# Optimization experiments

Hardware: AMD Instinct MI355X
Metric: run time of the kernel (lower is better)

Reference implementation:

```python
import jax, jax.numpy as jnp
import numpy as np

D_MODEL = 512
D_STATE = 16
D_CONV = 4
D_INNER = 2 * D_MODEL          # expand = 2 (mamba_ssm default)
DT_RANK = (D_MODEL + 15) // 16  # ceil(d_model/16) = 32
B, L = 2, 2048


def setup_inputs() -> dict:
    key = jax.random.key(0)
    ks = jax.random.split(key, 12)
    s = lambda k, shp, sc: jax.random.normal(k, shp, jnp.float32) * sc
    return {
        "x": s(ks[0], (B, L, D_MODEL), 1.0),
        "context": s(ks[1], (B, L, D_MODEL), 1.0),
        # Mamba params
        "in_proj_w": s(ks[2], (2 * D_INNER, D_MODEL), 0.02),
        "conv_w": s(ks[3], (D_INNER, D_CONV), 0.2),        # depthwise conv kernel
        "conv_b": jnp.zeros((D_INNER,), jnp.float32),
        "x_proj_w": s(ks[4], (DT_RANK + 2 * D_STATE, D_INNER), 0.02),
        "dt_proj_w": s(ks[5], (D_INNER, DT_RANK), 0.1),
        "dt_proj_b": s(ks[6], (D_INNER,), 0.1),
        "A_log": jnp.log(jnp.tile(jnp.arange(1, D_STATE + 1, dtype=jnp.float32), (D_INNER, 1))),
        "D": jnp.ones((D_INNER,), jnp.float32),
        "out_proj_w": s(ks[7], (D_MODEL, D_INNER), 0.02),
        # context gate params
        "gate_w": s(ks[8], (D_MODEL, 2 * D_MODEL), 0.02),
        "gate_b": jnp.zeros((D_MODEL,), jnp.float32),
    }


def _mamba(x, in_proj_w, conv_w, conv_b, x_proj_w, dt_proj_w, dt_proj_b, A_log, D, out_proj_w):
    Bsz, Ln, _ = x.shape
    # input projection -> [B, L, 2*E], split into ssm branch xi and gate z
    xz = jnp.einsum('bld,ed->ble', x, in_proj_w)
    xi, z = jnp.split(xz, 2, axis=-1)
    # causal depthwise conv1d (kernel D_CONV) + SiLU
    xp = jnp.pad(xi, ((0, 0), (D_CONV - 1, 0), (0, 0)))
    xc = sum(xp[:, k:k + Ln, :] * conv_w[:, k] for k in range(D_CONV)) + conv_b
    xc = jax.nn.silu(xc)
    # input-dependent dt, B, C
    dbc = jnp.einsum('ble,fe->blf', xc, x_proj_w)
    dt, Bm, Cm = jnp.split(dbc, [DT_RANK, DT_RANK + D_STATE], axis=-1)
    dt = jax.nn.softplus(jnp.einsum('blr,er->ble', dt, dt_proj_w) + dt_proj_b)  # [B,L,E]
    A = -jnp.exp(A_log)                                   # [E,S]
    dA = jnp.exp(dt[..., None] * A)                       # [B,L,E,S]
    dBx = dt[..., None] * Bm[:, :, None, :] * xc[..., None]  # [B,L,E,S]

    def step(h, ins):
        dA_t, dBx_t, C_t = ins
        h = dA_t * h + dBx_t                              # [B,E,S]
        y = jnp.einsum('bes,bs->be', h, C_t)
        return h, y

    h0 = jnp.zeros((Bsz, D_INNER, D_STATE), x.dtype)
    _, ys = jax.lax.scan(step, h0,
                         (dA.transpose(1, 0, 2, 3), dBx.transpose(1, 0, 2, 3), Cm.transpose(1, 0, 2)))
    y = ys.transpose(1, 0, 2) + xc * D                    # skip term D*x
    y = y * jax.nn.silu(z)                                # gated output
    return jnp.einsum('ble,de->bld', y, out_proj_w)


def reference(x, context, in_proj_w, conv_w, conv_b, x_proj_w, dt_proj_w, dt_proj_b,
              A_log, D, out_proj_w, gate_w, gate_b):
    m = _mamba(x, in_proj_w, conv_w, conv_b, x_proj_w, dt_proj_w, dt_proj_b, A_log, D, out_proj_w)
    g_in = jnp.concatenate([m, context], axis=-1)         # [B,L,2*d_model]
    gate = jax.nn.sigmoid(jnp.einsum('ble,de->bld', g_in, gate_w) + gate_b)
    return m * gate
```

## Files before the change

kernel.cpp:

```cpp
#include <hip/hip_runtime.h>
#include <cstdint>
#include <cstddef>

#define B_SZ   2
#define L_SZ   2048
#define BL     (B_SZ * L_SZ)
#define DMODEL 512
#define DINNER 1024
#define DSTATE 16
#define DTRANK 32
#define DTROWS 16
#define NCH    16
#define CHL    (L_SZ / NCH)

typedef unsigned short u16;
typedef __attribute__((ext_vector_type(8))) short          bf16x8;
typedef __attribute__((ext_vector_type(8))) unsigned short u16x8;
typedef __attribute__((ext_vector_type(4))) float          f32x4;

__device__ __forceinline__ void gload16(const void* g, void* l) {
    __builtin_amdgcn_global_load_lds(
        (const __attribute__((address_space(1))) unsigned int*)g,
        (__attribute__((address_space(3))) unsigned int*)l, 16, 0, 0);
}

__device__ __forceinline__ u16 bf16_rne(float x) {
    unsigned u = __float_as_uint(x);
    return (u16)((u + 0x7fffu + ((u >> 16) & 1u)) >> 16);
}

__global__ __launch_bounds__(256) void cvt_hl_k(
    const float* __restrict__ src, u16* __restrict__ hi, u16* __restrict__ lo,
    int shift, int dst_stride, int col_off)
{
    const long long base = ((long long)blockIdx.x * 256 + threadIdx.x) * 8;
    const long long row  = base >> shift;
    const int       col  = (int)(base & ((1 << shift) - 1));
    float4 f0 = *(const float4*)(src + base);
    float4 f1 = *(const float4*)(src + base + 4);
    float f[8] = {f0.x, f0.y, f0.z, f0.w, f1.x, f1.y, f1.z, f1.w};
    u16x8 h8, l8;
#pragma unroll
    for (int i = 0; i < 8; ++i) {
        u16 hb = bf16_rne(f[i]);
        float hf = __uint_as_float((unsigned)hb << 16);
        h8[i] = hb;
        l8[i] = bf16_rne(f[i] - hf);
    }
    const long long d = row * dst_stride + col_off + col;
    *(u16x8*)(hi + d) = h8;
    *(u16x8*)(lo + d) = l8;
}

template<int NF, int EPI>
__global__ __launch_bounds__(256) void gemm_bf16hl(
    const u16* __restrict__ Ah, const u16* __restrict__ Al,
    const u16* __restrict__ Wh, const u16* __restrict__ Wl,
    const float* __restrict__ bias, const float* __restrict__ Mul,
    float* __restrict__ C, float* __restrict__ C2, int M, int N, int K)
{
    constexpr int BN  = NF * 32;
    constexpr int NIB = BN / 16;
    constexpr int TOT = 16 + 2 * NIB;
    __shared__ u16 sAh[128][32], sAl[128][32];
    __shared__ u16 sBh[BN][32],  sBl[BN][32];

    const int tid  = threadIdx.x;
    const int w    = tid >> 6;
    const int lane = tid & 63;
    const int bm   = blockIdx.x * 128;
    const int bn   = blockIdx.y * BN;
    const int wm   = w >> 1;
    const int wn   = w & 1;
    const int lm   = lane & 15;
    const int lk8  = (lane >> 4) * 8;
    const int srow = lane >> 2;
    const int scol = (lane & 3) * 8;

    f32x4 acc[4][NF];
#pragma unroll
    for (int i = 0; i < 4; ++i)
#pragma unroll
        for (int j = 0; j < NF; ++j) acc[i][j] = (f32x4){0.f, 0.f, 0.f, 0.f};

    for (int k0 = 0; k0 < K; k0 += 32) {
        __syncthreads();
        for (int idx = w; idx < TOT; idx += 4) {
            const u16* gs; u16* ls;
            if (idx < 8)            { gs = Ah + (size_t)(bm + idx * 16 + srow) * K;              ls = &sAh[idx * 16][0]; }
            else if (idx < 16)      { gs = Al + (size_t)(bm + (idx - 8) * 16 + srow) * K;        ls = &sAl[(idx - 8) * 16][0]; }
            else if (idx < 16 + NIB){ gs = Wh + (size_t)(bn + (idx - 16) * 16 + srow) * K;       ls = &sBh[(idx - 16) * 16][0]; }
            else                    { gs = Wl + (size_t)(bn + (idx - 16 - NIB) * 16 + srow) * K; ls = &sBl[(idx - 16 - NIB) * 16][0]; }
            gload16(gs + k0 + scol, ls);
        }
        __syncthreads();

        bf16x8 a_h[4], a_l[4], b_h[NF], b_l[NF];
#pragma unroll
        for (int mi = 0; mi < 4; ++mi) {
            a_h[mi] = *(const bf16x8*)&sAh[wm * 64 + mi * 16 + lm][lk8];
            a_l[mi] = *(const bf16x8*)&sAl[wm * 64 + mi * 16 + lm][lk8];
        }
#pragma unroll
        for (int ni = 0; ni < NF; ++ni) {
            b_h[ni] = *(const bf16x8*)&sBh[wn * (NF * 16) + ni * 16 + lm][lk8];
            b_l[ni] = *(const bf16x8*)&sBl[wn * (NF * 16) + ni * 16 + lm][lk8];
        }
#pragma unroll
        for (int mi = 0; mi < 4; ++mi)
#pragma unroll
            for (int ni = 0; ni < NF; ++ni) {
                acc[mi][ni] = __builtin_amdgcn_mfma_f32_16x16x32_bf16(a_h[mi], b_h[ni], acc[mi][ni], 0, 0, 0);
                acc[mi][ni] = __builtin_amdgcn_mfma_f32_16x16x32_bf16(a_h[mi], b_l[ni], acc[mi][ni], 0, 0, 0);
                acc[mi][ni] = __builtin_amdgcn_mfma_f32_16x16x32_bf16(a_l[mi], b_h[ni], acc[mi][ni], 0, 0, 0);
            }
    }

    const int lr4 = (lane >> 4) * 4;
#pragma unroll
    for (int mi = 0; mi < 4; ++mi)
#pragma unroll
        for (int ni = 0; ni < NF; ++ni)
#pragma unroll
            for (int r = 0; r < 4; ++r) {
                const int row = bm + wm * 64 + mi * 16 + lr4 + r;
                const int col = bn + wn * (NF * 16) + ni * 16 + lm;
                if (EPI == 0) {
                    C[(size_t)row * N + col] = acc[mi][ni][r];
                } else if (EPI == 1) {
                    const size_t o = (size_t)row * N + col;
                    const float v = acc[mi][ni][r] + bias[col];
                    C[o] = Mul[o] / (1.f + expf(-v));
                } else {
                    if (col < DINNER) C [(size_t)row * DINNER + col]          = acc[mi][ni][r];
                    else              C2[(size_t)row * DINNER + col - DINNER] = acc[mi][ni][r];
                }
            }
}

__global__ __launch_bounds__(256) void gemm_xproj(
    const float* __restrict__ A, const float* __restrict__ W,
    float* __restrict__ C, int M, int N, int K)
{
    __shared__ float As[16][64];
    __shared__ float Ws[16][64];
    const int tid  = threadIdx.x;
    const int bm   = blockIdx.x * 64;
    const int tm   = (tid >> 4) * 4;
    const int tn   = (tid & 15) * 4;
    const int lrow = tid >> 2;
    const int lk   = (tid & 3) * 4;

    float acc[4][4];
#pragma unroll
    for (int i = 0; i < 4; ++i)
#pragma unroll
        for (int j = 0; j < 4; ++j) acc[i][j] = 0.f;

    for (int k0 = 0; k0 < K; k0 += 16) {
        const int kk = k0 + lk;
        float4 av = *(const float4*)(A + (size_t)(bm + lrow) * K + kk);
        float4 wv = *(const float4*)(W + (size_t)lrow * K + kk);
        __syncthreads();
        As[lk + 0][lrow] = av.x; As[lk + 1][lrow] = av.y;
        As[lk + 2][lrow] = av.z; As[lk + 3][lrow] = av.w;
        Ws[lk + 0][lrow] = wv.x; Ws[lk + 1][lrow] = wv.y;
        Ws[lk + 2][lrow] = wv.z; Ws[lk + 3][lrow] = wv.w;
        __syncthreads();
#pragma unroll
        for (int k = 0; k < 16; ++k) {
            float4 a4 = *(const float4*)&As[k][tm];
            float4 b4 = *(const float4*)&Ws[k][tn];
            float a[4] = {a4.x, a4.y, a4.z, a4.w};
            float b[4] = {b4.x, b4.y, b4.z, b4.w};
#pragma unroll
            for (int i = 0; i < 4; ++i)
#pragma unroll
                for (int j = 0; j < 4; ++j)
                    acc[i][j] = fmaf(a[i], b[j], acc[i][j]);
        }
    }
#pragma unroll
    for (int i = 0; i < 4; ++i)
        *(float4*)(C + (size_t)(bm + tm + i) * N + tn) =
            make_float4(acc[i][0], acc[i][1], acc[i][2], acc[i][3]);
}

__global__ __launch_bounds__(256) void conv_silu_k(
    const float* __restrict__ xi, const float* __restrict__ cw,
    const float* __restrict__ cb, float* __restrict__ xc)
{
    const int idx = blockIdx.x * 256 + threadIdx.x;
    const int e  = idx & (DINNER - 1);
    const int bl = idx >> 10;
    const int l  = bl & (L_SZ - 1);
    const float4 w = *(const float4*)(cw + e * 4);
    float acc = cb[e];
    acc = fmaf(xi[(size_t)bl * DINNER + e], w.w, acc);
    if (l >= 1) acc = fmaf(xi[(size_t)(bl - 1) * DINNER + e], w.z, acc);
    if (l >= 2) acc = fmaf(xi[(size_t)(bl - 2) * DINNER + e], w.y, acc);
    if (l >= 3) acc = fmaf(xi[(size_t)(bl - 3) * DINNER + e], w.x, acc);
    xc[idx] = acc / (1.f + expf(-acc));
}

__global__ __launch_bounds__(256) void dt_softplus_k(
    const float* __restrict__ dbc, const float* __restrict__ Wdt,
    const float* __restrict__ bdt, float* __restrict__ dt)
{
    __shared__ float r[DTROWS][DTRANK];
    const int rb  = blockIdx.x * DTROWS;
    const int tid = threadIdx.x;
    for (int i = tid; i < DTROWS * DTRANK; i += 256)
        r[i >> 5][i & 31] = dbc[(size_t)(rb + (i >> 5)) * 64 + (i & 31)];
    __syncthreads();
    for (int n = tid; n < DINNER; n += 256) {
        float4 wv[8];
        const float* w = Wdt + (size_t)n * DTRANK;
#pragma unroll
        for (int q = 0; q < 8; ++q) wv[q] = *(const float4*)(w + q * 4);
        const float bn_ = bdt[n];
#pragma unroll
        for (int row = 0; row < DTROWS; ++row) {
            float acc = bn_;
#pragma unroll
            for (int q = 0; q < 8; ++q) {
                acc = fmaf(wv[q].x, r[row][q * 4 + 0], acc);
                acc = fmaf(wv[q].y, r[row][q * 4 + 1], acc);
                acc = fmaf(wv[q].z, r[row][q * 4 + 2], acc);
                acc = fmaf(wv[q].w, r[row][q * 4 + 3], acc);
            }
            dt[(size_t)(rb + row) * DINNER + n] = (acc > 20.f) ? acc : log1pf(expf(acc));
        }
    }
}


__global__ __launch_bounds__(128) void scan_p1(
    const float* __restrict__ dtb, const float* __restrict__ xc,
    const float* __restrict__ dbc, const float* __restrict__ A_log,
    float* __restrict__ Pst, float* __restrict__ Hst)
{
    const int bid = blockIdx.x;
    const int c  = bid & (NCH - 1);
    const int eg = (bid >> 4) & 127;
    const int b  = bid >> 11;
    const int tid = threadIdx.x;
    const int el = tid >> 4, s = tid & 15;
    const int e  = eg * 8 + el;

    const float Av = -expf(A_log[e * DSTATE + s]);
    const size_t base = (size_t)b * L_SZ + c * CHL;
    float h = 0.f, P = 1.f;

    float dtv = dtb[base * DINNER + e];
    float xcv = xc [base * DINNER + e];
    float Bv  = dbc[base * 64 + DTRANK + s];
    for (int l = 0; l < CHL; ++l) {
        float dt_n = 0.f, xc_n = 0.f, B_n = 0.f;
        if (l + 1 < CHL) {
            const size_t r = base + l + 1;
            dt_n = dtb[r * DINNER + e];
            xc_n = xc [r * DINNER + e];
            B_n  = dbc[r * 64 + DTRANK + s];
        }
        const float dA = expf(dtv * Av);
        h = fmaf(dA, h, dtv * Bv * xcv);
        P *= dA;
        dtv = dt_n; xcv = xc_n; Bv = B_n;
    }
    const size_t off = (((size_t)c * B_SZ + b) * DINNER + e) * DSTATE + s;
    Pst[off] = P;
    Hst[off] = h;
}

__global__ __launch_bounds__(256) void scan_comb(
    const float* __restrict__ Pst, float* __restrict__ Hst)
{
    const int idx = blockIdx.x * 256 + threadIdx.x;
    float h = 0.f;
    for (int c = 0; c < NCH; ++c) {
        const size_t off = (size_t)c * (B_SZ * DINNER * DSTATE) + idx;
        const float P = Pst[off];
        const float H = Hst[off];
        Hst[off] = h;
        h = fmaf(P, h, H);
    }
}

__global__ __launch_bounds__(128) void scan_p2(
    const float* __restrict__ dtb, const float* __restrict__ xc,
    const float* __restrict__ z, const float* __restrict__ dbc,
    const float* __restrict__ A_log, const float* __restrict__ Dp,
    const float* __restrict__ H0,
    u16* __restrict__ y_hi, u16* __restrict__ y_lo)
{
    const int bid = blockIdx.x;
    const int c  = bid & (NCH - 1);
    const int eg = (bid >> 4) & 127;
    const int b  = bid >> 11;
    const int tid = threadIdx.x;
    const int el = tid >> 4, s = tid & 15;
    const int e  = eg * 8 + el;

    const float Av = -expf(A_log[e * DSTATE + s]);
    const float Dv = Dp[e];
    const size_t base = (size_t)b * L_SZ + c * CHL;
    float h = H0[(((size_t)c * B_SZ + b) * DINNER + e) * DSTATE + s];

    float dtv = dtb[base * DINNER + e];
    float xcv = xc [base * DINNER + e];
    float Bv  = dbc[base * 64 + DTRANK + s];
    float Cv  = dbc[base * 64 + DTRANK + DSTATE + s];
    float zv  = z  [base * DINNER + e];
    for (int l = 0; l < CHL; ++l) {
        float dt_n = 0.f, xc_n = 0.f, B_n = 0.f, C_n = 0.f, z_n = 0.f;
        if (l + 1 < CHL) {
            const size_t r = base + l + 1;
            dt_n = dtb[r * DINNER + e];
            xc_n = xc [r * DINNER + e];
            B_n  = dbc[r * 64 + DTRANK + s];
            C_n  = dbc[r * 64 + DTRANK + DSTATE + s];
            z_n  = z  [r * DINNER + e];
        }
        h = fmaf(expf(dtv * Av), h, dtv * Bv * xcv);
        float yp = h * Cv;
        yp += __shfl_xor(yp, 1, 16);
        yp += __shfl_xor(yp, 2, 16);
        yp += __shfl_xor(yp, 4, 16);
        yp += __shfl_xor(yp, 8, 16);
        if (s == 0) {
            const float sg = zv / (1.f + expf(-zv));
            const float yv = fmaf(xcv, Dv, yp) * sg;
            const u16 hb = bf16_rne(yv);
            const float hf = __uint_as_float((unsigned)hb << 16);
            const size_t o = (base + l) * DINNER + e;
            y_hi[o] = hb;
            y_lo[o] = bf16_rne(yv - hf);
        }
        dtv = dt_n; xcv = xc_n; Bv = B_n; Cv = C_n; zv = z_n;
    }
}

extern "C" void kernel_launch(void* const* d_in, const int* in_sizes, int n_in,
                              void* d_out, int out_size, void* d_ws, size_t ws_size,
                              hipStream_t stream)
{
    const float* x         = (const float*)d_in[0];
    const float* context   = (const float*)d_in[1];
    const float* in_proj_w = (const float*)d_in[2];
    const float* conv_w    = (const float*)d_in[3];
    const float* conv_b    = (const float*)d_in[4];
    const float* x_proj_w  = (const float*)d_in[5];
    const float* dt_proj_w = (const float*)d_in[6];
    const float* dt_proj_b = (const float*)d_in[7];
    const float* A_log     = (const float*)d_in[8];
    const float* Dvec      = (const float*)d_in[9];
    const float* out_proj_w= (const float*)d_in[10];
    const float* gate_w    = (const float*)d_in[11];
    const float* gate_b    = (const float*)d_in[12];
    float* out = (float*)d_out;

    char* wsb = (char*)d_ws;
    float* xi   = (float*)(wsb + (size_t)( 0u << 20));
    float* z    = (float*)(wsb + (size_t)(16u << 20));
    float* xc   = (float*)(wsb + (size_t)(32u << 20));
    float* dbc  = (float*)(wsb + (size_t)(48u << 20));
    float* dt   = (float*)(wsb + (size_t)(49u << 20));
    float* m    = (float*)(wsb + (size_t)(65u << 20));
    u16* x_hi   = (u16*)(wsb + (size_t)(65u << 20));
    u16* x_lo   = (u16*)(wsb + (size_t)(69u << 20));
    u16* Wi_hi  = (u16*)(wsb + (size_t)(73u << 20));
    u16* Wi_lo  = (u16*)(wsb + (size_t)(75u << 20));
    float* Pst  = (float*)(wsb + (size_t)(73u << 20));
    float* Hst  = (float*)(wsb + (size_t)(75u << 20));
    u16* Wo_hi  = (u16*)(wsb + (size_t)(77u << 20));
    u16* Wo_lo  = (u16*)(wsb + (size_t)(78u << 20));
    u16* Wg_hi  = (u16*)(wsb + (size_t)(79u << 20));
    u16* Wg_lo  = (u16*)(wsb + (size_t)(80u << 20));
    u16* y_hi   = (u16*)(wsb + (size_t)( 0u << 20));
    u16* y_lo   = (u16*)(wsb + (size_t)( 8u << 20));
    u16* A7_hi  = (u16*)(wsb + (size_t)(16u << 20));
    u16* A7_lo  = (u16*)(wsb + (size_t)(24u << 20));

    cvt_hl_k<<<1024, 256, 0, stream>>>(x,          x_hi,  x_lo,   9,  512, 0);
    cvt_hl_k<<< 512, 256, 0, stream>>>(in_proj_w,  Wi_hi, Wi_lo,  9,  512, 0);
    cvt_hl_k<<< 256, 256, 0, stream>>>(out_proj_w, Wo_hi, Wo_lo, 10, 1024, 0);
    cvt_hl_k<<< 256, 256, 0, stream>>>(gate_w,     Wg_hi, Wg_lo, 10, 1024, 0);
    gemm_bf16hl<4, 2><<<dim3(BL / 128, 2048 / 128), 256, 0, stream>>>(
        x_hi, x_lo, Wi_hi, Wi_lo, nullptr, nullptr, xi, z, BL, 2048, DMODEL);
    conv_silu_k<<<(BL * DINNER) / 256, 256, 0, stream>>>(xi, conv_w, conv_b, xc);
    gemm_xproj<<<dim3(BL / 64, 1), 256, 0, stream>>>(xc, x_proj_w, dbc, BL, 64, DINNER);
    dt_softplus_k<<<BL / DTROWS, 256, 0, stream>>>(dbc, dt_proj_w, dt_proj_b, dt);
    scan_p1<<<B_SZ * 128 * NCH, 128, 0, stream>>>(dt, xc, dbc, A_log, Pst, Hst);
    scan_comb<<<(B_SZ * DINNER * DSTATE) / 256, 256, 0, stream>>>(Pst, Hst);
    scan_p2<<<B_SZ * 128 * NCH, 128, 0, stream>>>(dt, xc, z, dbc, A_log, Dvec, Hst,
                                                  y_hi, y_lo);
    gemm_bf16hl<2, 0><<<dim3(BL / 128, DMODEL / 64), 256, 0, stream>>>(
        y_hi, y_lo, Wo_hi, Wo_lo, nullptr, nullptr, m, nullptr, BL, DMODEL, DINNER);
    cvt_hl_k<<<1024, 256, 0, stream>>>(m,       A7_hi, A7_lo, 9, 1024, 0);
    cvt_hl_k<<<1024, 256, 0, stream>>>(context, A7_hi, A7_lo, 9, 1024, DMODEL);
    gemm_bf16hl<2, 1><<<dim3(BL / 128, DMODEL / 64), 256, 0, stream>>>(
        A7_hi, A7_lo, Wg_hi, Wg_lo, gate_b, m, out, nullptr, BL, DMODEL, 2 * DMODEL);
}
```

Before: 484.6 us.

## Restructure chunked scan: 8 states per thread, more chunks, closed-form chunk decay

Rewrites both scan passes so each thread owns 8 state entries of one channel instead of one, with 128 channels per block. Loads of B and C become float4 vectors and the y reduction needs only one shuffle. The chunk count is doubled to keep the grid filled. Pass 1 computes the chunk decay product as exp2 of A times the summed dt rather than a running product, and exp is replaced by exp2 with a pre-scaled A. This cuts redundant per-lane loads of dt, xc and z and the shuffle work, at the cost of more registers per thread and twice the data for the combine step.

```diff
diff --git a/kernel.cpp b/kernel.cpp
--- a/kernel.cpp
+++ b/kernel.cpp
@@ -10,7 +10,7 @@
 #define DSTATE 16
 #define DTRANK 32
 #define DTROWS 16
-#define NCH    16
+#define NCH    32
 #define CHL    (L_SZ / NCH)
 
 typedef unsigned short u16;
@@ -235,42 +235,61 @@
 }
 
 
-__global__ __launch_bounds__(128) void scan_p1(
+__global__ __launch_bounds__(256) void scan_p1(
     const float* __restrict__ dtb, const float* __restrict__ xc,
     const float* __restrict__ dbc, const float* __restrict__ A_log,
     float* __restrict__ Pst, float* __restrict__ Hst)
 {
     const int bid = blockIdx.x;
-    const int c  = bid & (NCH - 1);
-    const int eg = (bid >> 4) & 127;
-    const int b  = bid >> 11;
+    const int c   = bid & (NCH - 1);
+    const int eg  = (bid >> 5) & 7;
+    const int b   = bid >> 8;
     const int tid = threadIdx.x;
-    const int el = tid >> 4, s = tid & 15;
-    const int e  = eg * 8 + el;
-
-    const float Av = -expf(A_log[e * DSTATE + s]);
-    const size_t base = (size_t)b * L_SZ + c * CHL;
-    float h = 0.f, P = 1.f;
-
-    float dtv = dtb[base * DINNER + e];
-    float xcv = xc [base * DINNER + e];
-    float Bv  = dbc[base * 64 + DTRANK + s];
+    const int e    = eg * 128 + (tid >> 1);
+    const int s0   = (tid & 1) * 8;
+
+    float A2[8];
+    {
+        float4 a0 = *(const float4*)(A_log + e * DSTATE + s0);
+        float4 a1 = *(const float4*)(A_log + e * DSTATE + s0 + 4);
+        const float c2 = 1.44269504088896f;
+        A2[0] = -expf(a0.x) * c2; A2[1] = -expf(a0.y) * c2;
+        A2[2] = -expf(a0.z) * c2; A2[3] = -expf(a0.w) * c2;
+        A2[4] = -expf(a1.x) * c2; A2[5] = -expf(a1.y) * c2;
+        A2[6] = -expf(a1.z) * c2; A2[7] = -expf(a1.w) * c2;
+    }
+    float h[8] = {0.f, 0.f, 0.f, 0.f, 0.f, 0.f, 0.f, 0.f};
+    float dtsum = 0.f;
+    const size_t base = (size_t)b * L_SZ + (size_t)c * CHL;
+    const float* dtp = dtb + base * DINNER + e;
+    const float* xcp = xc  + base * DINNER + e;
+    const float* dbp = dbc + base * 64 + DTRANK + s0;
+    float dtv = *dtp, xcv = *xcp;
+
     for (int l = 0; l < CHL; ++l) {
-        float dt_n = 0.f, xc_n = 0.f, B_n = 0.f;
-        if (l + 1 < CHL) {
-            const size_t r = base + l + 1;
-            dt_n = dtb[r * DINNER + e];
-            xc_n = xc [r * DINNER + e];
-            B_n  = dbc[r * 64 + DTRANK + s];
-        }
-        const float dA = expf(dtv * Av);
-        h = fmaf(dA, h, dtv * Bv * xcv);
-        P *= dA;
-        dtv = dt_n; xcv = xc_n; Bv = B_n;
-    }
-    const size_t off = (((size_t)c * B_SZ + b) * DINNER + e) * DSTATE + s;
-    Pst[off] = P;
-    Hst[off] = h;
+        float4 B0 = *(const float4*)(dbp);
+        float4 B1 = *(const float4*)(dbp + 4);
+        const size_t adv = (l + 1 < CHL) ? DINNER : 0;
+        float dt_n = dtp[adv];
+        float xc_n = xcp[adv];
+        dtsum += dtv;
+        const float u = dtv * xcv;
+        const float Bs[8] = {B0.x, B0.y, B0.z, B0.w, B1.x, B1.y, B1.z, B1.w};
+#pragma unroll
+        for (int j = 0; j < 8; ++j) {
+            const float dA = exp2f(dtv * A2[j]);
+            h[j] = fmaf(dA, h[j], Bs[j] * u);
+        }
+        dtv = dt_n; xcv = xc_n;
+        dtp += DINNER; xcp += DINNER; dbp += 64;
+    }
+    const size_t off = (((size_t)c * B_SZ + b) * DINNER + e) * DSTATE + s0;
+    *(float4*)(Pst + off)     = make_float4(exp2f(A2[0] * dtsum), exp2f(A2[1] * dtsum),
+                                            exp2f(A2[2] * dtsum), exp2f(A2[3] * dtsum));
+    *(float4*)(Pst + off + 4) = make_float4(exp2f(A2[4] * dtsum), exp2f(A2[5] * dtsum),
+                                            exp2f(A2[6] * dtsum), exp2f(A2[7] * dtsum));
+    *(float4*)(Hst + off)     = make_float4(h[0], h[1], h[2], h[3]);
+    *(float4*)(Hst + off + 4) = make_float4(h[4], h[5], h[6], h[7]);
 }
 
 __global__ __launch_bounds__(256) void scan_comb(
@@ -287,7 +306,7 @@
     }
 }
 
-__global__ __launch_bounds__(128) void scan_p2(
+__global__ __launch_bounds__(256) void scan_p2(
     const float* __restrict__ dtb, const float* __restrict__ xc,
     const float* __restrict__ z, const float* __restrict__ dbc,
     const float* __restrict__ A_log, const float* __restrict__ Dp,
@@ -295,49 +314,68 @@
     u16* __restrict__ y_hi, u16* __restrict__ y_lo)
 {
     const int bid = blockIdx.x;
-    const int c  = bid & (NCH - 1);
-    const int eg = (bid >> 4) & 127;
-    const int b  = bid >> 11;
+    const int c   = bid & (NCH - 1);
+    const int eg  = (bid >> 5) & 7;
+    const int b   = bid >> 8;
     const int tid = threadIdx.x;
-    const int el = tid >> 4, s = tid & 15;
-    const int e  = eg * 8 + el;
-
-    const float Av = -expf(A_log[e * DSTATE + s]);
+    const int e    = eg * 128 + (tid >> 1);
+    const int half = tid & 1;
+    const int s0   = half * 8;
+
+    float A2[8];
+    {
+        float4 a0 = *(const float4*)(A_log + e * DSTATE + s0);
+        float4 a1 = *(const float4*)(A_log + e * DSTATE + s0 + 4);
+        const float c2 = 1.44269504088896f;
+        A2[0] = -expf(a0.x) * c2; A2[1] = -expf(a0.y) * c2;
+        A2[2] = -expf(a0.z) * c2; A2[3] = -expf(a0.w) * c2;
+        A2[4] = -expf(a1.x) * c2; A2[5] = -expf(a1.y) * c2;
+        A2[6] = -expf(a1.z) * c2; A2[7] = -expf(a1.w) * c2;
+    }
     const float Dv = Dp[e];
-    const size_t base = (size_t)b * L_SZ + c * CHL;
-    float h = H0[(((size_t)c * B_SZ + b) * DINNER + e) * DSTATE + s];
-
-    float dtv = dtb[base * DINNER + e];
-    float xcv = xc [base * DINNER + e];
-    float Bv  = dbc[base * 64 + DTRANK + s];
-    float Cv  = dbc[base * 64 + DTRANK + DSTATE + s];
-    float zv  = z  [base * DINNER + e];
+    const size_t base = (size_t)b * L_SZ + (size_t)c * CHL;
+    const size_t hoff = (((size_t)c * B_SZ + b) * DINNER + e) * DSTATE + s0;
+    float h[8];
+    {
+        float4 h0 = *(const float4*)(H0 + hoff);
+        float4 h1 = *(const float4*)(H0 + hoff + 4);
+        h[0] = h0.x; h[1] = h0.y; h[2] = h0.z; h[3] = h0.w;
+        h[4] = h1.x; h[5] = h1.y; h[6] = h1.z; h[7] = h1.w;
+    }
+    const float* dtp = dtb + base * DINNER + e;
+    const float* xcp = xc  + base * DINNER + e;
+    const float* zp  = z   + base * DINNER + e;
+    const float* dbp = dbc + base * 64 + DTRANK + s0;
+    float dtv = *dtp, xcv = *xcp, zv = *zp;
+
     for (int l = 0; l < CHL; ++l) {
-        float dt_n = 0.f, xc_n = 0.f, B_n = 0.f, C_n = 0.f, z_n = 0.f;
-        if (l + 1 < CHL) {
-            const size_t r = base + l + 1;
-            dt_n = dtb[r * DINNER + e];
-            xc_n = xc [r * DINNER + e];
-            B_n  = dbc[r * 64 + DTRANK + s];
-            C_n  = dbc[r * 64 + DTRANK + DSTATE + s];
-            z_n  = z  [r * DINNER + e];
-        }
-        h = fmaf(expf(dtv * Av), h, dtv * Bv * xcv);
-        float yp = h * Cv;
-        yp += __shfl_xor(yp, 1, 16);
-        yp += __shfl_xor(yp, 2, 16);
-        yp += __shfl_xor(yp, 4, 16);
-        yp += __shfl_xor(yp, 8, 16);
-        if (s == 0) {
-            const float sg = zv / (1.f + expf(-zv));
-            const float yv = fmaf(xcv, Dv, yp) * sg;
-            const u16 hb = bf16_rne(yv);
-            const float hf = __uint_as_float((unsigned)hb << 16);
-            const size_t o = (base + l) * DINNER + e;
-            y_hi[o] = hb;
-            y_lo[o] = bf16_rne(yv - hf);
-        }
-        dtv = dt_n; xcv = xc_n; Bv = B_n; Cv = C_n; zv = z_n;
+        float4 B0 = *(const float4*)(dbp);
+        float4 B1 = *(const float4*)(dbp + 4);
+        float4 C0 = *(const float4*)(dbp + DSTATE);
+        float4 C1 = *(const float4*)(dbp + DSTATE + 4);
+        const size_t adv = (l + 1 < CHL) ? DINNER : 0;
+        float dt_n = dtp[adv];
+        float xc_n = xcp[adv];
+        float z_n  = zp[adv];
+        const float u = dtv * xcv;
+        const float Bs[8] = {B0.x, B0.y, B0.z, B0.w, B1.x, B1.y, B1.z, B1.w};
+        const float Cs[8] = {C0.x, C0.y, C0.z, C0.w, C1.x, C1.y, C1.z, C1.w};
+        float yp = 0.f;
+#pragma unroll
+        for (int j = 0; j < 8; ++j) {
+            const float dA = exp2f(dtv * A2[j]);
+            h[j] = fmaf(dA, h[j], Bs[j] * u);
+            yp = fmaf(h[j], Cs[j], yp);
+        }
+        yp += __shfl_xor(yp, 1);
+        const float sg = zv / (1.f + expf(-zv));
+        const float yv = fmaf(xcv, Dv, yp) * sg;
+        const u16 hb = bf16_rne(yv);
+        const size_t o = (base + l) * DINNER + e;
+        if (half == 0) y_hi[o] = hb;
+        else           y_lo[o] = bf16_rne(yv - __uint_as_float((unsigned)hb << 16));
+        dtv = dt_n; xcv = xc_n; zv = z_n;
+        dtp += DINNER; xcp += DINNER; zp += DINNER; dbp += 64;
     }
 }
 
@@ -369,10 +407,10 @@
     float* m    = (float*)(wsb + (size_t)(65u << 20));
     u16* x_hi   = (u16*)(wsb + (size_t)(65u << 20));
     u16* x_lo   = (u16*)(wsb + (size_t)(69u << 20));
+    float* Pst  = (float*)(wsb + (size_t)(65u << 20));
+    float* Hst  = (float*)(wsb + (size_t)(69u << 20));
     u16* Wi_hi  = (u16*)(wsb + (size_t)(73u << 20));
     u16* Wi_lo  = (u16*)(wsb + (size_t)(75u << 20));
-    float* Pst  = (float*)(wsb + (size_t)(73u << 20));
-    float* Hst  = (float*)(wsb + (size_t)(75u << 20));
     u16* Wo_hi  = (u16*)(wsb + (size_t)(77u << 20));
     u16* Wo_lo  = (u16*)(wsb + (size_t)(78u << 20));
     u16* Wg_hi  = (u16*)(wsb + (size_t)(79u << 20));
@@ -391,10 +429,10 @@
     conv_silu_k<<<(BL * DINNER) / 256, 256, 0, stream>>>(xi, conv_w, conv_b, xc);
     gemm_xproj<<<dim3(BL / 64, 1), 256, 0, stream>>>(xc, x_proj_w, dbc, BL, 64, DINNER);
     dt_softplus_k<<<BL / DTROWS, 256, 0, stream>>>(dbc, dt_proj_w, dt_proj_b, dt);
-    scan_p1<<<B_SZ * 128 * NCH, 128, 0, stream>>>(dt, xc, dbc, A_log, Pst, Hst);
+    scan_p1<<<B_SZ * 8 * NCH, 256, 0, stream>>>(dt, xc, dbc, A_log, Pst, Hst);
     scan_comb<<<(B_SZ * DINNER * DSTATE) / 256, 256, 0, stream>>>(Pst, Hst);
-    scan_p2<<<B_SZ * 128 * NCH, 128, 0, stream>>>(dt, xc, z, dbc, A_log, Dvec, Hst,
-                                                  y_hi, y_lo);
+    scan_p2<<<B_SZ * 8 * NCH, 256, 0, stream>>>(dt, xc, z, dbc, A_log, Dvec, Hst,
+                                                y_hi, y_lo);
     gemm_bf16hl<2, 0><<<dim3(BL / 128, DMODEL / 64), 256, 0, stream>>>(
         y_hi, y_lo, Wo_hi, Wo_lo, nullptr, nullptr, m, nullptr, BL, DMODEL, DINNER);
     cvt_hl_k<<<1024, 256, 0, stream>>>(m,       A7_hi, A7_lo, 9, 1024, 0);
```

New measurement: 405.6 us. 16.3% less time.
